# Kernel tuning notes

Measured on AMD Instinct MI355X. Metric: run time of the kernel, lower is better.

Reference implementation:

```python
import jax, jax.numpy as jnp
import numpy as np
from functools import partial

N = 100000
E = 1600000
F_IN, F_HID, F_OUT = 128, 128, 64


def setup_inputs() -> dict:
    key = jax.random.key(0)
    ks = jax.random.split(key, 10)
    x = jax.random.normal(ks[0], (N, F_IN), dtype=jnp.float32)
    edge_index = jax.random.randint(ks[1], (2, E), 0, N, dtype=jnp.int64)
    edge_attr = jax.random.uniform(ks[2], (E,), dtype=jnp.float32)
    # GCNConv params: Linear(in, out, bias=False) weight + separate bias
    def glorot(k, fan_in, fan_out):
        lim = jnp.sqrt(6.0 / (fan_in + fan_out))
        return jax.random.uniform(k, (fan_in, fan_out), minval=-lim, maxval=lim, dtype=jnp.float32)
    return {
        "x": x, "edge_index": edge_index, "edge_attr": edge_attr,
        "W1": glorot(ks[3], F_IN, F_HID),  "b1": jnp.zeros((F_HID,), jnp.float32),
        "W2": glorot(ks[4], F_HID, F_HID), "b2": jnp.zeros((F_HID,), jnp.float32),
        "W3": glorot(ks[5], F_HID, F_OUT), "b3": jnp.zeros((F_OUT,), jnp.float32),
    }


def _gcn_norm(src, dst, ew, n):
    # PyG gcn_norm: add self-loops with weight 1, symmetric normalization.
    loop = jnp.arange(n, dtype=src.dtype)
    src_f = jnp.concatenate([src, loop])
    dst_f = jnp.concatenate([dst, loop])
    ew_f = jnp.concatenate([ew, jnp.ones((n,), ew.dtype)])
    deg = jax.ops.segment_sum(ew_f, dst_f, num_segments=n)
    dinv = jnp.where(deg > 0, jax.lax.rsqrt(deg), 0.0)
    norm = dinv[src_f] * ew_f * dinv[dst_f]  # [E+N]
    return src_f, dst_f, norm


def _gcn_conv(x, W, b, src_f, dst_f, norm, n):
    h = x @ W  # [N, out]
    msg = norm[:, None] * h[src_f]  # gather + per-edge scale
    out = jax.ops.segment_sum(msg, dst_f, num_segments=n)  # scatter-add
    return out + b


def reference(x, edge_index, edge_attr, W1, b1, W2, b2, W3, b3):
    n = x.shape[0]
    src, dst = edge_index[0], edge_index[1]
    src_f, dst_f, norm = _gcn_norm(src, dst, edge_attr, n)
    h = jax.nn.relu(_gcn_conv(x, W1, b1, src_f, dst_f, norm, n))
    h = jax.nn.relu(_gcn_conv(h, W2, b2, src_f, dst_f, norm, n))
    out = _gcn_conv(h, W3, b3, src_f, dst_f, norm, n)
    return jax.nn.log_softmax(out, axis=-1)
```

## Files before the change

### kernel.cpp

```cpp
#include <hip/hip_runtime.h>

typedef unsigned short ushortT;
typedef unsigned int uintT;
typedef unsigned long long ullT;
typedef __attribute__((ext_vector_type(8))) short bf16x8;
typedef __attribute__((ext_vector_type(4))) float f32x4;

#define NBUCK 391
#define EPB   2048
#define NBEB  782

union H16 { ushortT u; _Float16 h; };

__device__ __forceinline__ float bf2f(uintT u16) {
    return __uint_as_float(u16 << 16);
}
__device__ __forceinline__ ushortT f2bf(float f) {
    unsigned int u = __float_as_uint(f);
    unsigned int r = (u + 0x7fffu + ((u >> 16) & 1u)) >> 16;
    return (ushortT)r;
}


__device__ __forceinline__ void twist_body(const float* W, ushortT* Wt, int K, int C, int idx) {
    if (idx < K * C) {
        int k = idx / C, c = idx - k * C;
        Wt[c * K + k] = f2bf(W[idx]);
    }
}

template <int C, bool ABF16>
__device__ __forceinline__ void gemm_body(const void* Aop, const ushortT* Wt,
                                          ushortT* outp, int nrows, int bid, int tid) {
    const int K = 128;
    int wv = tid >> 6;
    int ln = tid & 63;
    int row0 = (bid * 4 + wv) * 16;
    if (row0 >= nrows) return;
    int rA = ln & 15;
    int kg = ln >> 4;
    int rowA = row0 + rA;
    bool okA = rowA < nrows;

    bf16x8 af[4];
    if (ABF16) {
        const ushortT* A = (const ushortT*)Aop;
        #pragma unroll
        for (int kb = 0; kb < 4; ++kb) {
            if (okA) af[kb] = *(const bf16x8*)(A + (size_t)rowA * K + kb * 32 + kg * 8);
            else     af[kb] = (bf16x8)(short)0;
        }
    } else {
        const float* A = (const float*)Aop;
        #pragma unroll
        for (int kb = 0; kb < 4; ++kb) {
            bf16x8 t = (bf16x8)(short)0;
            if (okA) {
                const float4* ap = reinterpret_cast<const float4*>(A + (size_t)rowA * K + kb * 32 + kg * 8);
                float4 p0 = ap[0], p1 = ap[1];
                t[0] = (short)f2bf(p0.x); t[1] = (short)f2bf(p0.y);
                t[2] = (short)f2bf(p0.z); t[3] = (short)f2bf(p0.w);
                t[4] = (short)f2bf(p1.x); t[5] = (short)f2bf(p1.y);
                t[6] = (short)f2bf(p1.z); t[7] = (short)f2bf(p1.w);
            }
            af[kb] = t;
        }
    }

    int colB = ln & 15;
    f32x4 acc[C / 16];
    #pragma unroll
    for (int nt = 0; nt < C / 16; ++nt) acc[nt] = (f32x4)0.0f;
    #pragma unroll
    for (int nt = 0; nt < C / 16; ++nt) {
        int c = nt * 16 + colB;
        #pragma unroll
        for (int kb = 0; kb < 4; ++kb) {
            bf16x8 bfr = *(const bf16x8*)(Wt + c * K + kb * 32 + kg * 8);
            acc[nt] = __builtin_amdgcn_mfma_f32_16x16x32_bf16(af[kb], bfr, acc[nt], 0, 0, 0);
        }
    }
    #pragma unroll
    for (int nt = 0; nt < C / 16; ++nt) {
        #pragma unroll
        for (int r = 0; r < 4; ++r) {
            int rowC = row0 + (ln >> 4) * 4 + r;
            if (rowC < nrows) outp[(size_t)rowC * C + nt * 16 + colB] = f2bf(acc[nt][r]);
        }
    }
}

__global__ __launch_bounds__(256) void k_hist_twist(const int* dst, int* bucket_count,
                                                    int* blockbase, int e,
                                                    const float* W1, ushortT* Wt1,
                                                    const float* W2, ushortT* Wt2,
                                                    const float* W3, ushortT* Wt3) {
    __shared__ int hist[NBUCK];
    int blk = blockIdx.x, t = threadIdx.x;
    if (blk < NBEB) {
        for (int b = t; b < NBUCK; b += 256) hist[b] = 0;
        __syncthreads();
        int base = blk * EPB;
        for (int j = t; j < EPB; j += 256) {
            int i = base + j;
            if (i < e) atomicAdd(&hist[dst[i] >> 8], 1);
        }
        __syncthreads();
        for (int b = t; b < NBUCK; b += 256) {
            int h = hist[b];
            int old = 0;
            if (h > 0) old = atomicAdd(&bucket_count[b], h);
            blockbase[blk * NBUCK + b] = old;
        }
    } else {
        int tb = blk - NBEB;
        if (tb < 64)       twist_body(W1, Wt1, 128, 128, tb * 256 + t);
        else if (tb < 128) twist_body(W2, Wt2, 128, 128, (tb - 64) * 256 + t);
        else               twist_body(W3, Wt3, 128, 64, (tb - 128) * 256 + t);
    }
}

__global__ __launch_bounds__(512) void k_scanb(const int* bucket_count, int* bucket_base) {
    __shared__ int lds[512];
    int t = threadIdx.x;
    int v = (t < NBUCK) ? bucket_count[t] : 0;
    lds[t] = v; __syncthreads();
    for (int off = 1; off < 512; off <<= 1) {
        int x = 0; if (t >= off) x = lds[t - off];
        __syncthreads();
        if (t >= off) lds[t] += x;
        __syncthreads();
    }
    if (t < NBUCK) bucket_base[t] = (t == 0) ? 0 : lds[t - 1];
}

__global__ __launch_bounds__(256) void k_scatter_gemm1(const int* src, const int* dst,
                                                       const float* ew,
                                                       const int* bucket_base, const int* blockbase,
                                                       ullT* erec, int e,
                                                       const float* x, const ushortT* Wt1,
                                                       ushortT* hw1, int n) {
    __shared__ int hist[NBUCK];
    __shared__ int basec[NBUCK];
    int blk = blockIdx.x, t = threadIdx.x;
    if (blk < NBEB) {
        for (int b = t; b < NBUCK; b += 256) {
            hist[b] = 0;
            basec[b] = bucket_base[b] + blockbase[blk * NBUCK + b];
        }
        __syncthreads();
        int base = blk * EPB;
        for (int j = t; j < EPB; j += 256) {
            int i = base + j;
            if (i < e) {
                int d = dst[i];
                int b = d >> 8;
                int rank = atomicAdd(&hist[b], 1);
                H16 cv; cv.h = (_Float16)ew[i];
                ullT rec = ((ullT)(uintT)src[i] << 24) | ((ullT)(uintT)(d & 255) << 16) | (ullT)cv.u;
                erec[(size_t)basec[b] + rank] = rec;
            }
        }
    } else {
        gemm_body<128, false>(x, Wt1, hw1, n, blk - NBEB, t);
    }
}

__global__ __launch_bounds__(512) void k_bucket(const ullT* erec, const int* bucket_base,
                                                const int* bucket_count,
                                                uintT* entries, float* dinv, int* counts, int n) {
    __shared__ int cnt[256];
    __shared__ uintT wsum[256];
    int b = blockIdx.x, t = threadIdx.x;
    if (t < 256) { cnt[t] = 0; wsum[t] = 0; }
    __syncthreads();
    int beg = bucket_base[b], m = bucket_count[b];
    for (int j = t; j < m; j += 512) {
        ullT rec = erec[(size_t)beg + j];
        int dlow = (int)((rec >> 16) & 255);
        ushortT hu = (ushortT)(rec & 0xffffu);
        int slot = atomicAdd(&cnt[dlow], 1);
        H16 cv; cv.u = hu;
        atomicAdd(&wsum[dlow], (uintT)__float2uint_rn((float)cv.h * 16777216.0f));
        if (slot < 64) {
            uintT s = (uintT)(rec >> 24);
            entries[((size_t)b * 256 + dlow) * 64 + slot] = (s << 15) | (uintT)hu;
        }
    }
    __syncthreads();
    int node = b * 256 + t;
    if (t < 256 && node < n) {
        float sum = (float)wsum[t] * (1.0f / 16777216.0f);
        dinv[node] = rsqrtf(1.0f + sum);
        int c = cnt[t];
        counts[node] = c > 64 ? 64 : c;
    }
}

template <int C, bool ABF16>
__global__ __launch_bounds__(256) void k_gemm(const void* Aop, const ushortT* Wt,
                                              ushortT* outp, int nrows) {
    gemm_body<C, ABF16>(Aop, Wt, outp, nrows, blockIdx.x, threadIdx.x);
}

__global__ __launch_bounds__(256) void k_agg128(const char* hwb, const float* dinv,
                                                const int* counts, const uintT* entries,
                                                const float* bias, uintT* outp, int n) {
    __shared__ ullT wp[4][64];
    int wv = threadIdx.x >> 6, ln = threadIdx.x & 63;
    int i = blockIdx.x * 4 + wv;
    if (i >= n) return;

    float wfac = dinv[i];
    int cnt = counts[i];
    int cntp = (cnt + 7) & ~7;
    uintT ent = entries[(size_t)i * 64 + ln];
    int s_l = (ln < cnt) ? (int)(ent >> 15) : 0;
    H16 cv; cv.u = (ushortT)(ent & 0x7fffu);
    float w_l = (ln < cnt) ? dinv[s_l] * (float)cv.h * wfac : 0.f;
    wp[wv][ln] = ((ullT)__float_as_uint(w_l) << 32) | (ullT)((uintT)s_l << 8);

    const char* lane_base = hwb + (size_t)ln * 4;
    uintT us = *(const uintT*)(lane_base + (size_t)i * 256);
    float selfw = wfac * wfac;
    float acc0 = selfw * bf2f(us & 0xffffu);
    float acc1 = selfw * bf2f(us >> 16);

    for (int e = 0; e < cntp; e += 8) {
        ullT p0 = wp[wv][e + 0], p1 = wp[wv][e + 1], p2 = wp[wv][e + 2], p3 = wp[wv][e + 3];
        ullT p4 = wp[wv][e + 4], p5 = wp[wv][e + 5], p6 = wp[wv][e + 6], p7 = wp[wv][e + 7];
        uintT u0 = *(const uintT*)(lane_base + (uintT)p0);
        uintT u1 = *(const uintT*)(lane_base + (uintT)p1);
        uintT u2 = *(const uintT*)(lane_base + (uintT)p2);
        uintT u3 = *(const uintT*)(lane_base + (uintT)p3);
        uintT u4 = *(const uintT*)(lane_base + (uintT)p4);
        uintT u5 = *(const uintT*)(lane_base + (uintT)p5);
        uintT u6 = *(const uintT*)(lane_base + (uintT)p6);
        uintT u7 = *(const uintT*)(lane_base + (uintT)p7);
        float w0 = __uint_as_float((uintT)(p0 >> 32)), w1 = __uint_as_float((uintT)(p1 >> 32));
        float w2 = __uint_as_float((uintT)(p2 >> 32)), w3 = __uint_as_float((uintT)(p3 >> 32));
        float w4 = __uint_as_float((uintT)(p4 >> 32)), w5 = __uint_as_float((uintT)(p5 >> 32));
        float w6 = __uint_as_float((uintT)(p6 >> 32)), w7 = __uint_as_float((uintT)(p7 >> 32));
        acc0 += w0 * bf2f(u0 & 0xffffu); acc1 += w0 * bf2f(u0 >> 16);
        acc0 += w1 * bf2f(u1 & 0xffffu); acc1 += w1 * bf2f(u1 >> 16);
        acc0 += w2 * bf2f(u2 & 0xffffu); acc1 += w2 * bf2f(u2 >> 16);
        acc0 += w3 * bf2f(u3 & 0xffffu); acc1 += w3 * bf2f(u3 >> 16);
        acc0 += w4 * bf2f(u4 & 0xffffu); acc1 += w4 * bf2f(u4 >> 16);
        acc0 += w5 * bf2f(u5 & 0xffffu); acc1 += w5 * bf2f(u5 >> 16);
        acc0 += w6 * bf2f(u6 & 0xffffu); acc1 += w6 * bf2f(u6 >> 16);
        acc0 += w7 * bf2f(u7 & 0xffffu); acc1 += w7 * bf2f(u7 >> 16);
    }
    float2 bs = *(const float2*)(bias + 2 * ln);
    acc0 = fmaxf(acc0 + bs.x, 0.f);
    acc1 = fmaxf(acc1 + bs.y, 0.f);
    outp[(size_t)i * 64 + ln] = (uintT)f2bf(acc0) | ((uintT)f2bf(acc1) << 16);
}

__global__ __launch_bounds__(256) void k_agg_softmax(const char* hwb, const float* dinv,
                                                     const int* counts, const uintT* entries,
                                                     const float* bias, float* outp, int n) {
    __shared__ ullT wp[4][64];
    int wv = threadIdx.x >> 6, ln = threadIdx.x & 63;
    int i = blockIdx.x * 4 + wv;
    if (i >= n) return;

    float wfac = dinv[i];
    int cnt = counts[i];
    int cntp = (cnt + 7) & ~7;
    uintT ent = entries[(size_t)i * 64 + ln];
    int s_l = (ln < cnt) ? (int)(ent >> 15) : 0;
    H16 cv; cv.u = (ushortT)(ent & 0x7fffu);
    float w_l = (ln < cnt) ? dinv[s_l] * (float)cv.h * wfac : 0.f;
    wp[wv][ln] = ((ullT)__float_as_uint(w_l) << 32) | (ullT)((uintT)s_l << 7);

    const char* lane_base = hwb + (size_t)ln * 2;
    H16 sv; sv.u = *(const ushortT*)(lane_base + (size_t)i * 128);
    float acc = wfac * wfac * bf2f(sv.u);

    for (int e = 0; e < cntp; e += 8) {
        ullT p0 = wp[wv][e + 0], p1 = wp[wv][e + 1], p2 = wp[wv][e + 2], p3 = wp[wv][e + 3];
        ullT p4 = wp[wv][e + 4], p5 = wp[wv][e + 5], p6 = wp[wv][e + 6], p7 = wp[wv][e + 7];
        ushortT h0 = *(const ushortT*)(lane_base + (uintT)p0);
        ushortT h1 = *(const ushortT*)(lane_base + (uintT)p1);
        ushortT h2 = *(const ushortT*)(lane_base + (uintT)p2);
        ushortT h3 = *(const ushortT*)(lane_base + (uintT)p3);
        ushortT h4 = *(const ushortT*)(lane_base + (uintT)p4);
        ushortT h5 = *(const ushortT*)(lane_base + (uintT)p5);
        ushortT h6 = *(const ushortT*)(lane_base + (uintT)p6);
        ushortT h7 = *(const ushortT*)(lane_base + (uintT)p7);
        acc += __uint_as_float((uintT)(p0 >> 32)) * bf2f(h0);
        acc += __uint_as_float((uintT)(p1 >> 32)) * bf2f(h1);
        acc += __uint_as_float((uintT)(p2 >> 32)) * bf2f(h2);
        acc += __uint_as_float((uintT)(p3 >> 32)) * bf2f(h3);
        acc += __uint_as_float((uintT)(p4 >> 32)) * bf2f(h4);
        acc += __uint_as_float((uintT)(p5 >> 32)) * bf2f(h5);
        acc += __uint_as_float((uintT)(p6 >> 32)) * bf2f(h6);
        acc += __uint_as_float((uintT)(p7 >> 32)) * bf2f(h7);
    }
    acc += bias[ln];
    float m = acc;
    #pragma unroll
    for (int off = 32; off; off >>= 1) m = fmaxf(m, __shfl_xor(m, off));
    float ex = __expf(acc - m);
    float sm = ex;
    #pragma unroll
    for (int off = 32; off; off >>= 1) sm += __shfl_xor(sm, off);
    float r = acc - m - __logf(sm);
    outp[(size_t)i * 64 + ln] = r;
}

extern "C" void kernel_launch(void* const* d_in, const int* in_sizes, int n_in,
                              void* d_out, int out_size, void* d_ws, size_t ws_size,
                              hipStream_t stream) {
    const int N = 100000, E = 1600000;
    const int NPAD = NBUCK * 256;
    const float* x  = (const float*)d_in[0];
    const int*   src = (const int*)d_in[1];
    const int*   dst = src + E;
    const float* ea = (const float*)d_in[2];
    const float* W1 = (const float*)d_in[3];
    const float* b1 = (const float*)d_in[4];
    const float* W2 = (const float*)d_in[5];
    const float* b2 = (const float*)d_in[6];
    const float* W3 = (const float*)d_in[7];
    const float* b3 = (const float*)d_in[8];
    float* outp = (float*)d_out;

    char* ws = (char*)d_ws;
    auto alloc = [&](size_t bytes) {
        char* p = ws;
        ws += (bytes + 255) & ~(size_t)255;
        return p;
    };
    int*   bucket_count = (int*)alloc((size_t)NBUCK * 4);
    int*   bucket_base  = (int*)alloc((size_t)NBUCK * 4);
    int*   blockbase    = (int*)alloc((size_t)NBEB * NBUCK * 4);
    ullT*  erec         = (ullT*)alloc((size_t)E * 8);
    float* dinv    = (float*)alloc((size_t)N * 4);
    int*   counts  = (int*)  alloc((size_t)N * 4);
    uintT* entries = (uintT*)alloc((size_t)NPAD * 64 * 4);
    ushortT* Wt1   = (ushortT*)alloc(128 * 128 * 2);
    ushortT* Wt2   = (ushortT*)alloc(128 * 128 * 2);
    ushortT* Wt3   = (ushortT*)alloc(128 * 64 * 2);
    ushortT* hwA   = (ushortT*)alloc((size_t)N * 128 * 2);
    ushortT* hwB   = (ushortT*)alloc((size_t)N * 128 * 2);

    const int nbGemm = (N + 63) / 64;
    const int nbAgg  = (N + 3) / 4;

    hipMemsetAsync(bucket_count, 0, (size_t)NBUCK * 4, stream);
    k_hist_twist<<<NBEB + 160, 256, 0, stream>>>(dst, bucket_count, blockbase, E,
                                                 W1, Wt1, W2, Wt2, W3, Wt3);
    k_scanb<<<1, 512, 0, stream>>>(bucket_count, bucket_base);
    k_scatter_gemm1<<<NBEB + nbGemm, 256, 0, stream>>>(src, dst, ea, bucket_base, blockbase,
                                                       erec, E, x, Wt1, hwA, N);
    k_bucket<<<NBUCK, 512, 0, stream>>>(erec, bucket_base, bucket_count,
                                        entries, dinv, counts, N);

    k_agg128<<<nbAgg, 256, 0, stream>>>((const char*)hwA, dinv, counts, entries,
                                        b1, (uintT*)hwB, N);
    k_gemm<128, true><<<nbGemm, 256, 0, stream>>>(hwB, Wt2, hwA, N);
    k_agg128<<<nbAgg, 256, 0, stream>>>((const char*)hwA, dinv, counts, entries,
                                        b2, (uintT*)hwB, N);
    k_gemm<64, true><<<nbGemm, 256, 0, stream>>>(hwB, Wt3, hwA, N);
    k_agg_softmax<<<nbAgg, 256, 0, stream>>>((const char*)hwA, dinv, counts, entries,
                                             b3, outp, N);
}
```

Baseline: 427.2 us.

## Stage edge records in LDS for coalesced scatter; fuse GEMM1 with bucket pass

The scatter kernel now processes 4096 edges per block. It counting-sorts the records by bucket in LDS with a local prefix scan, then writes them to global memory in sorted order so the stores are mostly contiguous instead of random. The first-layer GEMM moves from the scatter kernel into the bucket kernel, which now runs 256 threads per block. The aim is fewer scattered global writes and better overlap of GEMM1 with the bucket pass. The cost is extra LDS use (about 50KB per block), more barriers, and half as many scatter blocks.

```diff
diff --git a/kernel.cpp b/kernel.cpp
--- a/kernel.cpp
+++ b/kernel.cpp
@@ -7,8 +7,8 @@
 typedef __attribute__((ext_vector_type(4))) float f32x4;
 
 #define NBUCK 391
-#define EPB   2048
-#define NBEB  782
+#define EPB   4096
+#define NBEB  391
 
 union H16 { ushortT u; _Float16 h; };
 
@@ -134,66 +134,87 @@
     if (t < NBUCK) bucket_base[t] = (t == 0) ? 0 : lds[t - 1];
 }
 
-__global__ __launch_bounds__(256) void k_scatter_gemm1(const int* src, const int* dst,
-                                                       const float* ew,
-                                                       const int* bucket_base, const int* blockbase,
-                                                       ullT* erec, int e,
-                                                       const float* x, const ushortT* Wt1,
-                                                       ushortT* hw1, int n) {
-    __shared__ int hist[NBUCK];
-    __shared__ int basec[NBUCK];
+__global__ __launch_bounds__(512) void k_scatter(const int* src, const int* dst, const float* ew,
+                                                 const int* bucket_base, const int* blockbase,
+                                                 ullT* erec, int e) {
+    __shared__ ullT srec[EPB];
+    __shared__ int  gaddr[EPB];
+    __shared__ int  hist[512];
+    __shared__ int  adj[NBUCK];
     int blk = blockIdx.x, t = threadIdx.x;
-    if (blk < NBEB) {
-        for (int b = t; b < NBUCK; b += 256) {
-            hist[b] = 0;
-            basec[b] = bucket_base[b] + blockbase[blk * NBUCK + b];
-        }
-        __syncthreads();
-        int base = blk * EPB;
-        for (int j = t; j < EPB; j += 256) {
-            int i = base + j;
-            if (i < e) {
-                int d = dst[i];
-                int b = d >> 8;
-                int rank = atomicAdd(&hist[b], 1);
-                H16 cv; cv.h = (_Float16)ew[i];
-                ullT rec = ((ullT)(uintT)src[i] << 24) | ((ullT)(uintT)(d & 255) << 16) | (ullT)cv.u;
-                erec[(size_t)basec[b] + rank] = rec;
-            }
-        }
-    } else {
-        gemm_body<128, false>(x, Wt1, hw1, n, blk - NBEB, t);
-    }
-}
-
-__global__ __launch_bounds__(512) void k_bucket(const ullT* erec, const int* bucket_base,
-                                                const int* bucket_count,
-                                                uintT* entries, float* dinv, int* counts, int n) {
+    hist[t] = 0;
+    __syncthreads();
+    int base = blk * EPB;
+    for (int j = t; j < EPB; j += 512) {
+        int i = base + j;
+        if (i < e) atomicAdd(&hist[dst[i] >> 8], 1);
+    }
+    __syncthreads();
+    for (int off = 1; off < 512; off <<= 1) {
+        int x = 0; if (t >= off) x = hist[t - off];
+        __syncthreads();
+        if (t >= off) hist[t] += x;
+        __syncthreads();
+    }
+    int lb = (t == 0) ? 0 : hist[t - 1];
+    __syncthreads();
+    hist[t] = lb;
+    if (t < NBUCK) adj[t] = bucket_base[t] + blockbase[blk * NBUCK + t] - lb;
+    __syncthreads();
+    for (int j = t; j < EPB; j += 512) {
+        int i = base + j;
+        if (i < e) {
+            int d = dst[i];
+            int b = d >> 8;
+            int pos = atomicAdd(&hist[b], 1);
+            H16 cv; cv.h = (_Float16)ew[i];
+            ullT rec = ((ullT)(uintT)src[i] << 24) | ((ullT)(uintT)(d & 255) << 16) | (ullT)cv.u;
+            srec[pos] = rec;
+            gaddr[pos] = adj[b] + pos;
+        }
+    }
+    __syncthreads();
+    int m = e - base; if (m > EPB) m = EPB;
+    for (int k = t; k < m; k += 512) {
+        erec[(size_t)gaddr[k]] = srec[k];
+    }
+}
+
+__global__ __launch_bounds__(256) void k_bucket_gemm1(const ullT* erec, const int* bucket_base,
+                                                      const int* bucket_count,
+                                                      uintT* entries, float* dinv, int* counts, int n,
+                                                      const float* x, const ushortT* Wt1,
+                                                      ushortT* hw1) {
     __shared__ int cnt[256];
     __shared__ uintT wsum[256];
-    int b = blockIdx.x, t = threadIdx.x;
-    if (t < 256) { cnt[t] = 0; wsum[t] = 0; }
-    __syncthreads();
-    int beg = bucket_base[b], m = bucket_count[b];
-    for (int j = t; j < m; j += 512) {
-        ullT rec = erec[(size_t)beg + j];
-        int dlow = (int)((rec >> 16) & 255);
-        ushortT hu = (ushortT)(rec & 0xffffu);
-        int slot = atomicAdd(&cnt[dlow], 1);
-        H16 cv; cv.u = hu;
-        atomicAdd(&wsum[dlow], (uintT)__float2uint_rn((float)cv.h * 16777216.0f));
-        if (slot < 64) {
-            uintT s = (uintT)(rec >> 24);
-            entries[((size_t)b * 256 + dlow) * 64 + slot] = (s << 15) | (uintT)hu;
-        }
-    }
-    __syncthreads();
-    int node = b * 256 + t;
-    if (t < 256 && node < n) {
-        float sum = (float)wsum[t] * (1.0f / 16777216.0f);
-        dinv[node] = rsqrtf(1.0f + sum);
-        int c = cnt[t];
-        counts[node] = c > 64 ? 64 : c;
+    int blk = blockIdx.x, t = threadIdx.x;
+    if (blk < NBUCK) {
+        int b = blk;
+        cnt[t] = 0; wsum[t] = 0;
+        __syncthreads();
+        int beg = bucket_base[b], m = bucket_count[b];
+        for (int j = t; j < m; j += 256) {
+            ullT rec = erec[(size_t)beg + j];
+            int dlow = (int)((rec >> 16) & 255);
+            ushortT hu = (ushortT)(rec & 0xffffu);
+            int slot = atomicAdd(&cnt[dlow], 1);
+            H16 cv; cv.u = hu;
+            atomicAdd(&wsum[dlow], (uintT)__float2uint_rn((float)cv.h * 16777216.0f));
+            if (slot < 64) {
+                uintT s = (uintT)(rec >> 24);
+                entries[((size_t)b * 256 + dlow) * 64 + slot] = (s << 15) | (uintT)hu;
+            }
+        }
+        __syncthreads();
+        int node = b * 256 + t;
+        if (node < n) {
+            float sum = (float)wsum[t] * (1.0f / 16777216.0f);
+            dinv[node] = rsqrtf(1.0f + sum);
+            int c = cnt[t];
+            counts[node] = c > 64 ? 64 : c;
+        }
+    } else {
+        gemm_body<128, false>(x, Wt1, hw1, n, blk - NBUCK, t);
     }
 }
 
@@ -352,11 +373,10 @@
     k_hist_twist<<<NBEB + 160, 256, 0, stream>>>(dst, bucket_count, blockbase, E,
                                                  W1, Wt1, W2, Wt2, W3, Wt3);
     k_scanb<<<1, 512, 0, stream>>>(bucket_count, bucket_base);
-    k_scatter_gemm1<<<NBEB + nbGemm, 256, 0, stream>>>(src, dst, ea, bucket_base, blockbase,
-                                                       erec, E, x, Wt1, hwA, N);
-    k_bucket<<<NBUCK, 512, 0, stream>>>(erec, bucket_base, bucket_count,
-                                        entries, dinv, counts, N);
-
+    k_scatter<<<NBEB, 512, 0, stream>>>(src, dst, ea, bucket_base, blockbase, erec, E);
+    k_bucket_gemm1<<<NBUCK + nbGemm, 256, 0, stream>>>(erec, bucket_base, bucket_count,
+                                                       entries, dinv, counts, N,
+                                                       x, Wt1, hwA);
     k_agg128<<<nbAgg, 256, 0, stream>>>((const char*)hwA, dinv, counts, entries,
                                         b1, (uintT*)hwB, N);
     k_gemm<128, true><<<nbGemm, 256, 0, stream>>>(hwB, Wt2, hwA, N);
```

Result: faster. 414.4 us (-3.0%).
